# Kernel optimization log

Hardware: AMD Instinct MI355X
Metric: run time of the kernel (lower is better)

The kernel has to match this reference:

```python
import jax, jax.numpy as jnp
import numpy as np

MUL = 128            # channel multiplicity (node feature channels)
Z = 10               # number of chemical elements (node_attrs dim)
L_DIMS = (1, 3, 5, 7)   # edge SH irrep dims, lmax=3
MM_DIMS = (1, 3)        # magmom SH irrep dims, lmax=1
AVG_NUM_NEIGHBORS = 20.0
N_NODES = 5000
N_EDGES = 100000
R_DIM = 8            # edge radial feature dim
MM_INV_DIM = 8       # magmom invariant feature dim


def _mlp(x, Ws, act):
    # e3nn FullyConnectedNet: variance-preserving linear layers, act between hidden layers
    for W in Ws[:-1]:
        h = x @ W * (1.0 / np.sqrt(W.shape[0]))
        x = act(h) if act is not None else h
    return x @ Ws[-1] * (1.0 / np.sqrt(Ws[-1].shape[0]))


def _conv_tp(x, sh, w, dims):
    # channelwise 'uvu' tensor product: (MUL x 0e) x SH(l) -> MUL x l per l.
    # x:[E,MUL], sh:[E,sum(dims)], w:[E,MUL,n_l]. CG for 0e x l -> l is trivial.
    outs, off = [], 0
    for l, d in enumerate(dims):
        blk = (w[:, :, l] * x)[:, :, None] * sh[:, None, off:off + d]  # [E,MUL,d]
        outs.append(blk.reshape(x.shape[0], MUL * d))
        off += d
    return jnp.concatenate(outs, axis=-1)


def _per_l_linear(x, Ws, dims):
    # e3nn o3.Linear: per-l channel mixing with 1/sqrt(fan_in) normalization
    outs, off = [], 0
    scale = 1.0 / np.sqrt(MUL)
    for l, d in enumerate(dims):
        blk = x[:, off:off + MUL * d].reshape(-1, MUL, d)
        outs.append((jnp.einsum('nud,uv->nvd', blk, Ws[l]) * scale).reshape(-1, MUL * d))
        off += MUL * d
    return jnp.concatenate(outs, axis=-1)


def _skip_tp(x, attrs, Ws, dims):
    # FullyConnectedTensorProduct(irreps_out, Zx0e, irreps_out): per-l bilinear mix
    outs, off = [], 0
    scale = 1.0 / np.sqrt(MUL * attrs.shape[-1])
    for l, d in enumerate(dims):
        blk = x[:, off:off + MUL * d].reshape(-1, MUL, d)
        outs.append((jnp.einsum('nud,nz,uzv->nvd', blk, attrs, Ws[l]) * scale).reshape(-1, MUL * d))
        off += MUL * d
    return jnp.concatenate(outs, axis=-1)


def _reshape_irreps(x, dims):
    # [N, sum(MUL*d)] -> [N, MUL, sum(d)]
    outs, off = [], 0
    for d in dims:
        outs.append(x[:, off:off + MUL * d].reshape(-1, MUL, d))
        off += MUL * d
    return jnp.concatenate(outs, axis=-1)


def setup_inputs() -> dict:
    key = jax.random.key(0)
    ks = jax.random.split(key, 24)
    E, N = N_EDGES, N_NODES
    inp = {
        'node_attrs': jax.random.uniform(ks[0], (N, Z), jnp.float32),
        'node_feats': jax.random.normal(ks[1], (N, MUL), jnp.float32),
        'edge_attrs': jax.random.normal(ks[2], (E, sum(L_DIMS)), jnp.float32),
        'edge_feats': jax.random.uniform(ks[3], (E, R_DIM), jnp.float32),
        'magmom_node_inv_feats': jax.random.normal(ks[4], (N, MM_INV_DIM), jnp.float32),
        'magmom_node_attrs': jax.random.normal(ks[5], (N, sum(MM_DIMS)), jnp.float32),
        'edge_index': jax.random.randint(ks[6], (2, E), 0, N),
    }
    rin = R_DIM + MM_INV_DIM
    inp['W_up'] = jax.random.normal(ks[7], (MUL, MUL), jnp.float32)
    inp['W_rad1'] = jax.random.normal(ks[8], (rin, 64), jnp.float32)
    inp['W_rad2'] = jax.random.normal(ks[9], (64, 64), jnp.float32)
    inp['W_rad3'] = jax.random.normal(ks[10], (64, 64), jnp.float32)
    inp['W_rad4'] = jax.random.normal(ks[11], (64, MUL * len(L_DIMS)), jnp.float32)  # weight_numel=512
    inp['M_rad1'] = jax.random.normal(ks[12], (rin, 64), jnp.float32)
    inp['M_rad2'] = jax.random.normal(ks[13], (64, 64), jnp.float32)
    inp['M_rad3'] = jax.random.normal(ks[14], (64, 64), jnp.float32)
    inp['M_rad4'] = jax.random.normal(ks[15], (64, MUL * len(MM_DIMS)), jnp.float32)  # weight_numel=256
    inp['W_density'] = jax.random.normal(ks[16], (R_DIM, 1), jnp.float32)
    inp['W_lin'] = jax.random.normal(ks[17], (len(L_DIMS), MUL, MUL), jnp.float32)
    inp['W_mlin'] = jax.random.normal(ks[18], (len(MM_DIMS), MUL, MUL), jnp.float32)
    inp['W_skip'] = jax.random.normal(ks[19], (len(L_DIMS), MUL, Z, MUL), jnp.float32)
    inp['W_mskip'] = jax.random.normal(ks[20], (len(L_DIMS), MUL, Z, MUL), jnp.float32)
    return inp


def reference(node_attrs, node_feats, edge_attrs, edge_feats, magmom_node_inv_feats,
              magmom_node_attrs, W_up, W_rad1, W_rad2, W_rad3, W_rad4,
              M_rad1, M_rad2, M_rad3, M_rad4, W_density, W_lin, W_mlin,
              W_skip, W_mskip, edge_index):
    sender, receiver = edge_index[0], edge_index[1]
    E = edge_attrs.shape[0]
    N = node_feats.shape[0]
    silu = jax.nn.silu

    x = node_feats @ W_up * (1.0 / np.sqrt(MUL))  # linear_up
    xj = x[sender]                                # [E, MUL]
    ef_mm = jnp.concatenate([edge_feats, magmom_node_inv_feats[sender]], axis=-1)  # [E, 16]

    tp_w = _mlp(ef_mm, [W_rad1, W_rad2, W_rad3, W_rad4], silu)          # [E, 512]
    edge_density = jnp.tanh((edge_feats @ W_density * (1.0 / np.sqrt(R_DIM))) ** 2)  # [E, 1]

    w4 = tp_w.reshape(E, MUL, len(L_DIMS))
    pre_mji = _conv_tp(xj, edge_attrs, w4, L_DIMS)                      # [E, 2048]

    w_mm = _mlp(ef_mm, [M_rad1, M_rad2, M_rad3, M_rad4], None).reshape(E, MUL, len(MM_DIMS))
    w_mm = w_mm * pre_mji[:, :MUL][:, :, None]                          # density-gated by scalar part
    magmom_mji = _conv_tp(xj, magmom_node_attrs[sender], w_mm, MM_DIMS) # [E, 512]

    w4b = w4 * magmom_mji[:, :MUL][:, :, None]
    mji = _conv_tp(xj, edge_attrs, w4b, L_DIMS)                         # [E, 2048]

    density = jax.ops.segment_sum(edge_density, receiver, num_segments=N)  # [N, 1]
    msg = jax.ops.segment_sum(mji, receiver, num_segments=N)               # [N, 2048]
    mm_msg = jax.ops.segment_sum(magmom_mji, receiver, num_segments=N)     # [N, 512]

    msg = _per_l_linear(msg, W_lin, L_DIMS) / (density + 1.0)
    msg = _skip_tp(msg, node_attrs, W_skip, L_DIMS)

    mm = _per_l_linear(mm_msg, W_mlin, MM_DIMS) / AVG_NUM_NEIGHBORS
    # magmom_linear maps (128x0e+128x1o) -> target irreps: l=2,3 outputs have no path -> zero
    mm = jnp.concatenate([mm, jnp.zeros((N, MUL * (5 + 7)), mm.dtype)], axis=-1)
    mm = _skip_tp(mm, node_attrs, W_mskip, L_DIMS)

    out1 = _reshape_irreps(msg, L_DIMS)  # [N, 128, 16]
    out2 = _reshape_irreps(mm, L_DIMS)   # [N, 128, 16]
    return jnp.stack([out1, out2], axis=0)
```

## Files before the change

### kernel.cpp

```cpp
#include <hip/hip_runtime.h>
#include <stdint.h>


__device__ __forceinline__ float silu_f(float x) {
  return x / (1.0f + __expf(-x));
}

__global__ void k_zero_int(int* p, int n) {
  int i = blockIdx.x * blockDim.x + threadIdx.x;
  if (i < n) p[i] = 0;
}

__global__ __launch_bounds__(256) void k_prep(
    const float* __restrict__ M1, const float* __restrict__ M2,
    const float* __restrict__ M3, const float* __restrict__ M4,
    float* __restrict__ Mc) {
  __shared__ float T1[16 * 64];
  __shared__ float T2[16 * 64];
  int t = threadIdx.x;
  for (int i = t; i < 16 * 64; i += 256) {
    int r = i >> 6, c = i & 63;
    float s = 0.f;
    for (int k = 0; k < 64; k++) s += M1[r * 64 + k] * M2[k * 64 + c];
    T1[i] = s;
  }
// ... 56 lines not shown
    cursor[i] = base;
    base += deg[i];
  }
  if (t == 1023) rowstart[Nn] = part[1023];
}

__global__ void k_fill(const int* __restrict__ recv, int* __restrict__ cursor,
                       int* __restrict__ elist, int E) {
  int e = blockIdx.x * blockDim.x + threadIdx.x;
  if (e < E) {
    int p = atomicAdd(&cursor[recv[e]], 1);
    elist[p] = e;
  }
}

__global__ __launch_bounds__(256) void k_edge(
    const float* __restrict__ edge_feats, const float* __restrict__ mminv,
    const int* __restrict__ sender,
    const float* __restrict__ W1, const float* __restrict__ W2,
    const float* __restrict__ W3, const float* __restrict__ W4,
    const float* __restrict__ Mc, const float* __restrict__ Wd,
    float* __restrict__ w4e, float* __restrict__ wmme, float* __restrict__ dens,
    int E) {
  const int base = blockIdx.x * 8;
  const int t = threadIdx.x;
  __shared__ float ef[8][16];
  __shared__ float hA[8][64];
  __shared__ float hB[8][64];
  const int gwave = t >> 6;
  const int o6 = t & 63;

  if (t < 128) {
    int g = t >> 4, j = t & 15;
    int e = base + g;
    float v = 0.f;
    if (e < E) v = (j < 8) ? edge_feats[e * 8 + j] : mminv[sender[e] * 8 + (j - 8)];
    ef[g][j] = v;
  } else if (t < 136) {
    int g = t - 128;
    int e = base + g;
    if (e < E) {
      float q = 0.f;
#pragma unroll
      for (int k = 0; k < 8; k++) q += edge_feats[e * 8 + k] * Wd[k];
      q *= 0.35355339059327373f;
      dens[e] = tanhf(q * q);
    }
  }
  __syncthreads();

#pragma unroll
  for (int rep = 0; rep < 2; rep++) {
    int g = gwave + rep * 4;
    float s = 0.f;
#pragma unroll
    for (int k = 0; k < 16; k++) s += ef[g][k] * W1[k * 64 + o6];
// ... 31 lines not shown
    }
  }
  float c[8] = {0, 0, 0, 0, 0, 0, 0, 0};
#pragma unroll
  for (int k = 0; k < 16; k++) {
    float w = Mc[k * 256 + t];
#pragma unroll
    for (int g = 0; g < 8; g++) c[g] += ef[g][k] * w;
  }

  const int p0 = (t & 3) * 128 + (t >> 2);
  const int p1 = p0 + 64;
  const int pm = (t & 1) * 128 + (t >> 1);
#pragma unroll
  for (int g = 0; g < 8; g++) {
    int e = base + g;
    if (e < E) {
      w4e[(size_t)e * 512 + p0] = a[g] * 0.125f;
      w4e[(size_t)e * 512 + p1] = b[g] * 0.125f;
      wmme[(size_t)e * 256 + pm] = c[g];
    }
  }
}

__global__ __launch_bounds__(256) void k_edge_hA(
    const float* __restrict__ edge_feats, const float* __restrict__ mminv,
    const int* __restrict__ sender,
    const float* __restrict__ W1, const float* __restrict__ W2,
    const float* __restrict__ W3, const float* __restrict__ Wd,
    float* __restrict__ hAe, float* __restrict__ dens, int E) {
  const int base = blockIdx.x * 8;
  const int t = threadIdx.x;
  __shared__ float ef[8][16];
  __shared__ float hA[8][64];
  __shared__ float hB[8][64];
  const int gwave = t >> 6;
  const int o6 = t & 63;

  if (t < 128) {
    int g = t >> 4, j = t & 15;
    int e = base + g;
    float v = 0.f;
    if (e < E) v = (j < 8) ? edge_feats[e * 8 + j] : mminv[sender[e] * 8 + (j - 8)];
    ef[g][j] = v;
  } else if (t < 136) {
    int g = t - 128;
    int e = base + g;
    if (e < E) {
      float q = 0.f;
#pragma unroll
      for (int k = 0; k < 8; k++) q += edge_feats[e * 8 + k] * Wd[k];
      q *= 0.35355339059327373f;
      dens[e] = tanhf(q * q);
    }
  }
  __syncthreads();

#pragma unroll
  for (int rep = 0; rep < 2; rep++) {
    int g = gwave + rep * 4;
    float s = 0.f;
#pragma unroll
    for (int k = 0; k < 16; k++) s += ef[g][k] * W1[k * 64 + o6];
    hA[g][o6] = silu_f(s * 0.25f);
  }
#pragma unroll
  for (int rep = 0; rep < 2; rep++) {
    int g = gwave + rep * 4;
    float s = 0.f;
#pragma unroll 8
    for (int k = 0; k < 64; k++) s += hA[g][k] * W2[k * 64 + o6];
    hB[g][o6] = silu_f(s * 0.125f);
  }
#pragma unroll
  for (int rep = 0; rep < 2; rep++) {
    int g = gwave + rep * 4;
    float s = 0.f;
#pragma unroll 8
    for (int k = 0; k < 64; k++) s += hB[g][k] * W3[k * 64 + o6];
    int e = base + g;
    if (e < E) hAe[(size_t)e * 64 + o6] = silu_f(s * 0.125f);
  }
}

__global__ __launch_bounds__(256) void k_gather0(
    const float* __restrict__ x, const float* __restrict__ edge_attrs,
    const float* __restrict__ mmattrs, const int* __restrict__ sender,
    const float* __restrict__ w4e, const float* __restrict__ wmme,
    const float* __restrict__ dens,
    const int* __restrict__ rowstart, const int* __restrict__ elist,
    float* __restrict__ msg, float* __restrict__ mmr, float* __restrict__ densN,
    int Nn) {
  const int n = blockIdx.x;
  const int t = threadIdx.x;
  const int start = rowstart[n], end = rowstart[n + 1];

  __shared__ float shs[2][8][16];
  __shared__ float mmshs[2][8][4];

  float accm[8] = {0, 0, 0, 0, 0, 0, 0, 0};
  float accmm0 = 0.f, accmm1 = 0.f, accd = 0.f;
  const int u = t & 127;
  const int half = t >> 7;

  int erA[8], srA[8], erB[8], srB[8];
#pragma unroll
  for (int g = 0; g < 8; g++) { erA[g] = -1; srA[g] = 0; erB[g] = -1; srB[g] = 0; }

  if (start < end) {
    int idx = start + (t & 7);
    int v = (idx < end) ? elist[idx] : -1;
    int s = (v >= 0) ? sender[v] : 0;
    float d = (v >= 0) ? dens[v] : 0.f;
#pragma unroll
    for (int g = 0; g < 8; g++) {
      erA[g] = __shfl(v, g);
      srA[g] = __shfl(s, g);
      float dg = __shfl(d, g);
      if (t == 0) accd += dg;
    }
    if (t < 128) {
      int g = t >> 4, j = t & 15;
      shs[0][g][j] = (erA[g] >= 0) ? edge_attrs[erA[g] * 16 + j] : 0.f;
    } else if (t < 160) {
// ... 14 lines not shown
#pragma unroll
      for (int g = 0; g < 8; g++) {
        erB[g] = __shfl(v, g);
        srB[g] = __shfl(s, g);
        float dg = __shfl(d, g);
        if (t == 0) accd += dg;
      }
      if (t < 128) {
        int g = t >> 4, j = t & 15;
        shs[p ^ 1][g][j] = (erB[g] >= 0) ? edge_attrs[erB[g] * 16 + j] : 0.f;
      } else if (t < 160) {
        int g = (t - 128) >> 2, j = (t - 128) & 3;
        mmshs[p ^ 1][g][j] = (erB[g] >= 0) ? mmattrs[srB[g] * 4 + j] : 0.f;
      }
    }
#pragma unroll 2
    for (int g = 0; g < 8; g++) {
      if (erA[g] < 0) continue;
      const size_t b4 = (size_t)erA[g] * 512;
      const size_t bm = (size_t)erA[g] * 256;
      float w40 = w4e[b4 + u];
      float w41 = w4e[b4 + 128 + u];
      float w42 = w4e[b4 + 256 + u];
      float w43 = w4e[b4 + 384 + u];
      float wm0 = wmme[bm + u];
      float wm1 = wmme[bm + 128 + u];
      float xj = x[(size_t)srA[g] * 128 + u];
      float sh0 = shs[p][g][0];
      float pre0 = w40 * xj * sh0;
      float wg0 = wm0 * pre0;
      float wg1 = wm1 * pre0;
      float mm0 = wg0 * xj * mmshs[p][g][0];
      float m1 = wg1 * xj;
      float bx = mm0 * xj;
      float b0 = w40 * bx, b1 = w41 * bx, b2 = w42 * bx, b3 = w43 * bx;
      if (half == 0) {
        accmm0 += mm0;
        accmm1 += m1 * mmshs[p][g][1];
        accm[0] += b0 * sh0;
        accm[1] += b1 * shs[p][g][1];
        accm[2] += b1 * shs[p][g][2];
// ... 10 lines not shown
        accm[2] += b3 * shs[p][g][10];
        accm[3] += b3 * shs[p][g][11];
        accm[4] += b3 * shs[p][g][12];
        accm[5] += b3 * shs[p][g][13];
        accm[6] += b3 * shs[p][g][14];
        accm[7] += b3 * shs[p][g][15];
      }
    }
    __syncthreads();
    p ^= 1;
#pragma unroll
    for (int g = 0; g < 8; g++) { erA[g] = erB[g]; srA[g] = srB[g]; }
  }

  float4* mp = (float4*)(msg + (size_t)n * 2048 + u * 16 + half * 8);
  mp[0] = make_float4(accm[0], accm[1], accm[2], accm[3]);
  mp[1] = make_float4(accm[4], accm[5], accm[6], accm[7]);
  *(float2*)(mmr + (size_t)n * 512 + u * 4 + half * 2) = make_float2(accmm0, accmm1);
  if (t == 0) densN[n] = accd;
}

template <int D, int SP>
__device__ __forceinline__ void lin_body(
    const float* __restrict__ in, int in_rs, int in_us, int in_cb,
    const float* __restrict__ W, const float* __restrict__ densN, float basescl,
    bool useDinv, float* __restrict__ outp, int out_rs, int out_us, int out_cb,
    int Nn, int n0, float* lin_s) {
  const int t = threadIdx.x;
  for (int i = t; i < 16 * 128 * D; i += 256) {
    int nn = i / (128 * D);
    int r = i - nn * 128 * D;
    int uu = r / D;
    int m = r - uu * D;
    int nd = n0 + nn;
    lin_s[(nn * 128 + uu) * SP + m] =
        (nd < Nn) ? in[(size_t)nd * in_rs + uu * in_us + in_cb + m] : 0.f;
  }
  __syncthreads();

  const int v = t & 127, hf = t >> 7;
  float acc[8][D];
#pragma unroll
  for (int q = 0; q < 8; q++)
#pragma unroll
    for (int m = 0; m < D; m++) acc[q][m] = 0.f;

  for (int uu = 0; uu < 128; uu++) {
    float wv = W[uu * 128 + v];
#pragma unroll
    for (int q = 0; q < 8; q++) {
      const float* ls = &lin_s[((hf * 8 + q) * 128 + uu) * SP];
#pragma unroll
      for (int m = 0; m < D; m++) acc[q][m] += ls[m] * wv;
    }
  }
#pragma unroll
  for (int q = 0; q < 8; q++) {
    int nd = n0 + hf * 8 + q;
    if (nd < Nn) {
      float scl = basescl;
      if (useDinv) scl *= 1.0f / (densN[nd] + 1.0f);
      float* op = outp + (size_t)nd * out_rs + v * out_us + out_cb;
#pragma unroll
      for (int m = 0; m < D; m++) op[m] = acc[q][m] * scl;
    }
  }
}

__global__ __launch_bounds__(256) void k_lin(
    const float* __restrict__ msg, const float* __restrict__ mmr,
    const float* __restrict__ densN, const float* __restrict__ Wlin,
    const float* __restrict__ Wmlin, float* __restrict__ linm,
    float* __restrict__ linmm, int Nn) {
  __shared__ float lin_s[16 * 128 * 8];
  const int n0 = blockIdx.x * 16;
  const float scl = 0.08838834764831845f;
  const float sm = 0.08838834764831845f / 20.0f;
  switch (blockIdx.y) {
    case 0: lin_body<1, 1>(msg, 2048, 16, 0, Wlin, densN, scl, true, linm, 2048, 16, 0, Nn, n0, lin_s); break;
    case 1: lin_body<3, 4>(msg, 2048, 16, 1, Wlin + 16384, densN, scl, true, linm, 2048, 16, 1, Nn, n0, lin_s); break;
    case 2: lin_body<5, 8>(msg, 2048, 16, 4, Wlin + 32768, densN, scl, true, linm, 2048, 16, 4, Nn, n0, lin_s); break;
    case 3: lin_body<7, 8>(msg, 2048, 16, 9, Wlin + 49152, densN, scl, true, linm, 2048, 16, 9, Nn, n0, lin_s); break;
    case 4: lin_body<1, 1>(mmr, 512, 4, 0, Wmlin, densN, sm, false, linmm, 512, 4, 0, Nn, n0, lin_s); break;
    case 5: lin_body<3, 4>(mmr, 512, 4, 1, Wmlin + 16384, densN, sm, false, linmm, 512, 4, 1, Nn, n0, lin_s); break;
  }
}

template <int MODE>
__global__ __launch_bounds__(256) void k_gather_t(
    const float* __restrict__ x, const float* __restrict__ edge_attrs,
    const float* __restrict__ edge_feats, const float* __restrict__ mminv,
    const float* __restrict__ mmattrs, const int* __restrict__ sender,
    const float* __restrict__ W1, const float* __restrict__ W2,
    const float* __restrict__ W3, const float* __restrict__ W4,
    const float* __restrict__ Mc, const float* __restrict__ Wd,
    const float* __restrict__ dens, const float* __restrict__ hAe,
    const float* __restrict__ Wlin, const float* __restrict__ Wmlin,
    const int* __restrict__ rowstart, const int* __restrict__ elist,
    float* __restrict__ linm, float* __restrict__ linmm, int Nn) {
  const int n = blockIdx.x;
  const int t = threadIdx.x;
  const int start = rowstart[n], end = rowstart[n + 1];

  __shared__ float ef[8][16];
  __shared__ float hA[8][64];
  __shared__ float hB[8][64];
  __shared__ float ubuf[8 * 512 + 8 * 256];
  __shared__ float xjs[8][128];
  __shared__ float shs[8][16];
  __shared__ float mmshs[8][4];
  __shared__ float denss[8];
// ... 9 lines not shown
  float accmm0 = 0.f, accmm1 = 0.f;
  float accd = 0.f;

  const int u = t & 127;
  const int half = t >> 7;
  const int gwave = t >> 6;
  const int o6 = t & 63;

  for (int base = start; base < end; base += 8) {
    if (t < 8) {
      int g = t;
      if (base + g < end) {
        int e = elist[base + g];
        eS[g] = e;
        sS[g] = sender[e];
        if (MODE == 1) denss[g] = dens[e];
      } else {
        eS[g] = -1;
        sS[g] = 0;
        denss[g] = 0.f;
      }
    }
    __syncthreads();
    if (t < 128) {
      int g = t >> 4, j = t & 15;
      int e = eS[g];
      shs[g][j] = (e >= 0) ? edge_attrs[e * 16 + j] : 0.f;
      float v = 0.f;
      if (e >= 0) v = (j < 8) ? edge_feats[e * 8 + j] : mminv[sS[g] * 8 + (j - 8)];
      ef[g][j] = v;
    } else if (t < 160) {
      int g = (t - 128) >> 2, j = (t - 128) & 3;
      mmshs[g][j] = (eS[g] >= 0) ? mmattrs[sS[g] * 4 + j] : 0.f;
    }
    for (int i = t; i < 1024; i += 256) {
      int g = i >> 7, uu = i & 127;
      xjs[g][uu] = (eS[g] >= 0) ? x[sS[g] * 128 + uu] : 0.f;
    }
    if constexpr (MODE == 1) {
      for (int i = t; i < 512; i += 256) {
        int g = i >> 6, k = i & 63;
        hA[g][k] = (eS[g] >= 0) ? hAe[(size_t)eS[g] * 64 + k] : 0.f;
      }
    }
    if constexpr (MODE == 2) {
      if (t < 8 && eS[t] >= 0) {
        int e = eS[t];
        float q = 0.f;
#pragma unroll
        for (int k = 0; k < 8; k++) q += edge_feats[e * 8 + k] * Wd[k];
        q *= 0.35355339059327373f;
        denss[t] = tanhf(q * q);
      }
    }
    __syncthreads();

    if constexpr (MODE == 2) {
#pragma unroll
      for (int rep = 0; rep < 2; rep++) {
        int g = gwave + rep * 4;
        float s = 0.f;
#pragma unroll
        for (int k = 0; k < 16; k++) s += ef[g][k] * W1[k * 64 + o6];
        hA[g][o6] = silu_f(s * 0.25f);
      }
#pragma unroll
      for (int rep = 0; rep < 2; rep++) {
        int g = gwave + rep * 4;
        float s = 0.f;
#pragma unroll 8
        for (int k = 0; k < 64; k++) s += hA[g][k] * W2[k * 64 + o6];
        hB[g][o6] = silu_f(s * 0.125f);
      }
#pragma unroll
      for (int rep = 0; rep < 2; rep++) {
        int g = gwave + rep * 4;
        float s = 0.f;
#pragma unroll 8
        for (int k = 0; k < 64; k++) s += hB[g][k] * W3[k * 64 + o6];
        hA[g][o6] = silu_f(s * 0.125f);
      }
      __syncthreads();
    }

    {
      float a[8] = {0, 0, 0, 0, 0, 0, 0, 0};
      float b[8] = {0, 0, 0, 0, 0, 0, 0, 0};
#pragma unroll 8
      for (int k = 0; k < 64; k++) {
        float w0 = W4[k * 512 + t];
        float w1 = W4[k * 512 + t + 256];
#pragma unroll
        for (int g = 0; g < 8; g++) {
          float h = hA[g][k];
          a[g] += h * w0;
          b[g] += h * w1;
        }
      }
      int p0 = (t & 3) * 128 + (t >> 2);
// ... 5 lines not shown
      }
    }
    {
      float c[8] = {0, 0, 0, 0, 0, 0, 0, 0};
#pragma unroll
      for (int k = 0; k < 16; k++) {
        float w = Mc[k * 256 + t];
#pragma unroll
        for (int g = 0; g < 8; g++) c[g] += ef[g][k] * w;
      }
      int p = (t & 1) * 128 + (t >> 1);
#pragma unroll
      for (int g = 0; g < 8; g++) wmms[g][p] = c[g];
    }
    __syncthreads();

#pragma unroll 2
    for (int g = 0; g < 8; g++) {
      float w40 = w4s[g][u];
      float w41 = w4s[g][128 + u];
      float w42 = w4s[g][256 + u];
      float w43 = w4s[g][384 + u];
      float wm0 = wmms[g][u];
      float wm1 = wmms[g][128 + u];
      float xj = xjs[g][u];
      float sh0 = shs[g][0];
      float pre0 = w40 * xj * sh0;
      float wg0 = wm0 * pre0;
      float wg1 = wm1 * pre0;
      float mm0 = wg0 * xj * mmshs[g][0];
      float m1 = wg1 * xj;
      float bx = mm0 * xj;
      float b0 = w40 * bx, b1 = w41 * bx, b2 = w42 * bx, b3 = w43 * bx;
      if (half == 0) {
        accmm0 += mm0;
        accmm1 += m1 * mmshs[g][1];
        accm[0] += b0 * sh0;
        accm[1] += b1 * shs[g][1];
        accm[2] += b1 * shs[g][2];
        accm[3] += b1 * shs[g][3];
        accm[4] += b2 * shs[g][4];
        accm[5] += b2 * shs[g][5];
        accm[6] += b2 * shs[g][6];
        accm[7] += b2 * shs[g][7];
// ... 42 lines not shown
    }
  } else {
    for (int uu = 0; uu < 128; uu++) {
      float wl2 = Wlin[32768 + uu * 128 + u];
      float wl3 = Wlin[49152 + uu * 128 + u];
      outl[0] += msg_s[uu][8] * wl2;
      outl[1] += msg_s[uu][9] * wl3;
      outl[2] += msg_s[uu][10] * wl3;
      outl[3] += msg_s[uu][11] * wl3;
      outl[4] += msg_s[uu][12] * wl3;
      outl[5] += msg_s[uu][13] * wl3;
      outl[6] += msg_s[uu][14] * wl3;
      outl[7] += msg_s[uu][15] * wl3;
    }
  }
  const float scl = 0.08838834764831845f * dinv;
  float4 v0 = make_float4(outl[0] * scl, outl[1] * scl, outl[2] * scl, outl[3] * scl);
  float4 v1 = make_float4(outl[4] * scl, outl[5] * scl, outl[6] * scl, outl[7] * scl);
  float4* lp = (float4*)(linm + (size_t)n * 2048 + u * 16 + half * 8);
  lp[0] = v0;
  lp[1] = v1;

  float om0 = 0.f, om1 = 0.f;
  if (half == 0) {
    for (int uu = 0; uu < 128; uu++) {
      om0 += mm_s[uu][0] * Wmlin[uu * 128 + u];
      om1 += mm_s[uu][1] * Wmlin[16384 + uu * 128 + u];
    }
  } else {
    for (int uu = 0; uu < 128; uu++) {
      float wm1 = Wmlin[16384 + uu * 128 + u];
      om0 += mm_s[uu][2] * wm1;
      om1 += mm_s[uu][3] * wm1;
    }
  }
  const float sm = 0.08838834764831845f / 20.0f;
  *(float2*)(linmm + (size_t)n * 512 + u * 4 + half * 2) = make_float2(om0 * sm, om1 * sm);
}

__global__ void k_zero2(float* __restrict__ out2, int Nn) {
  int i = blockIdx.x * blockDim.x + threadIdx.x;
  if (i < Nn * 128) {
    float4 z = make_float4(0.f, 0.f, 0.f, 0.f);
    float4* p = (float4*)(out2 + (size_t)i * 16);
    p[1] = z;
    p[2] = z;
    p[3] = z;
  }
}

__global__ __launch_bounds__(128) void k_wt(const float* __restrict__ Wskip,
                                            const float* __restrict__ Wmskip,
                                            float* __restrict__ Wt) {
  int bx = blockIdx.x;
  int L = bx >> 7, u = bx & 127;
  int v = threadIdx.x;
  const float* src = (L < 4) ? (Wskip + (size_t)L * 163840)
                             : (Wmskip + (size_t)(L - 4) * 163840);
  float* dst = Wt + (((size_t)L * 128 + u) * 128 + v) * 12;
#pragma unroll
  for (int z = 0; z < 10; z++) dst[z] = src[u * 1280 + z * 128 + v];
  dst[10] = 0.f;
  dst[11] = 0.f;
}

template <int D, int SP>
__device__ __forceinline__ void skip_body2(
    const float* __restrict__ attrs, const float* __restrict__ in, int in_rs,
    int in_us, int in_cb, const float* __restrict__ Wt, float* __restrict__ outp,
    int out_cb, int Nn, int n0, float* lin_s, float (*attrs_s)[10]) {
  const int t = threadIdx.x;
  for (int i = t; i < 160; i += 256) {
    int nn = i / 10, z = i - nn * 10;
    int n = n0 + nn;
    attrs_s[nn][z] = (n < Nn) ? attrs[n * 10 + z] : 0.f;
  }
  for (int i = t; i < 16 * 128 * D; i += 256) {
    int nn = i / (128 * D);
// ... 85 lines not shown
  const float* M2 = (const float*)d_in[13];
  const float* M3 = (const float*)d_in[14];
  const float* M4 = (const float*)d_in[15];
  const float* Wd = (const float*)d_in[16];
  const float* Wlin = (const float*)d_in[17];
  const float* Wmlin = (const float*)d_in[18];
  const float* Wskip = (const float*)d_in[19];
  const float* Wmskip = (const float*)d_in[20];

  const int N = in_sizes[1] / 128;
  const int E = in_sizes[2] / 16;
  const int* sender = edge_index;
  const int* recv = edge_index + E;

  float* ws = (float*)d_ws;
  float* x = ws;   ws += (size_t)N * 128;
  float* Mc = ws;  ws += 16 * 256;
  float* Wt = ws;  ws += (size_t)6 * 128 * 128 * 12;

  const size_t intWords = (size_t)(N + 1) + N + N + E;
  const size_t headBytes = (size_t)((char*)ws - (char*)d_ws);
  const size_t needA = headBytes +
      ((size_t)N * 2048 + (size_t)N * 512 + N + intWords +
       (size_t)E * 512 + (size_t)E * 256 + E) * 4 + 64;
  const size_t needB = headBytes +
      ((size_t)N * 2048 + (size_t)N * 512 + (size_t)E * 64 + E + intWords) * 4 + 64;

  int mode;
  float *msg = nullptr, *mmr = nullptr, *densN = nullptr;
  float *w4e = nullptr, *wmme = nullptr, *dens = nullptr, *hAe = nullptr;
  float *linm = nullptr, *linmm = nullptr;
  int* ibuf = nullptr;

  if (ws_size >= needA) {
    mode = 0;
    msg = ws;   ws += (size_t)N * 2048;
    mmr = ws;   ws += (size_t)N * 512;
    densN = ws; ws += N;
    ibuf = (int*)ws;
    ws = (float*)(((uintptr_t)(ibuf + intWords) + 15) & ~(uintptr_t)15);
    w4e = ws;   ws += (size_t)E * 512;
    wmme = ws;  ws += (size_t)E * 256;
    dens = ws;  ws += E;
    linm = w4e;
    linmm = w4e + (size_t)N * 2048;
  } else if (ws_size >= needB) {
    mode = 1;
    linm = ws;  ws += (size_t)N * 2048;
    linmm = ws; ws += (size_t)N * 512;
    hAe = ws;   ws += (size_t)E * 64;
    dens = ws;  ws += E;
    ibuf = (int*)ws;
  } else {
    mode = 2;
    linm = ws;  ws += (size_t)N * 2048;
    linmm = ws; ws += (size_t)N * 512;
    ibuf = (int*)ws;
  }
  int* rowstart = ibuf;
  int* deg = ibuf + (N + 1);
  int* cursor = deg + N;
  int* elist = cursor + N;

  k_zero_int<<<(N + 255) / 256, 256, 0, stream>>>(deg, N);
  k_prep<<<1, 256, 0, stream>>>(M1, M2, M3, M4, Mc);
  k_wt<<<768, 128, 0, stream>>>(Wskip, Wmskip, Wt);
  k_up<<<N, 128, 0, stream>>>(node_feats, W_up, x, N);
  if (mode == 0) {
    k_edge<<<(E + 7) / 8, 256, 0, stream>>>(edge_feats, mminv, sender, W1, W2,
                                            W3, W4, Mc, Wd, w4e, wmme, dens, E);
  } else if (mode == 1) {
    k_edge_hA<<<(E + 7) / 8, 256, 0, stream>>>(edge_feats, mminv, sender, W1,
                                               W2, W3, Wd, hAe, dens, E);
  }
  k_count<<<(E + 255) / 256, 256, 0, stream>>>(recv, deg, E);
  k_scan<<<1, 1024, 0, stream>>>(deg, rowstart, cursor, N);
  k_fill<<<(E + 255) / 256, 256, 0, stream>>>(recv, cursor, elist, E);
  dim3 gs((N + 15) / 16, 6);
  if (mode == 0) {
    k_gather0<<<N, 256, 0, stream>>>(x, edge_attrs, mmattrs, sender, w4e, wmme,
                                     dens, rowstart, elist, msg, mmr, densN, N);
    k_lin<<<gs, 256, 0, stream>>>(msg, mmr, densN, Wlin, Wmlin, linm, linmm, N);
  } else if (mode == 1) {
    k_gather_t<1><<<N, 256, 0, stream>>>(x, edge_attrs, edge_feats, mminv,
                                         mmattrs, sender, W1, W2, W3, W4, Mc,
                                         Wd, dens, hAe, Wlin, Wmlin, rowstart,
                                         elist, linm, linmm, N);
  } else {
    k_gather_t<2><<<N, 256, 0, stream>>>(x, edge_attrs, edge_feats, mminv,
                                         mmattrs, sender, W1, W2, W3, W4, Mc,
                                         Wd, dens, hAe, Wlin, Wmlin, rowstart,
                                         elist, linm, linmm, N);
  }
  k_zero2<<<(N * 128 + 255) / 256, 256, 0, stream>>>((float*)d_out + (size_t)N * 2048, N);
  k_skip<<<gs, 256, 0, stream>>>(node_attrs, linm, linmm, Wt, (float*)d_out, N);
}
```

Baseline: 978.8 us.

## Compute edge weights in receiver-sorted segments and fuse linear into skip kernel

Edge weights are now computed in receiver-sorted order over segments sized to fit the workspace. A gather kernel runs per segment and accumulates into node buffers, replacing the earlier three workspace-dependent modes. The per-l linear is fused into the skip tensor-product kernel, which removes the intermediate linm/linmm buffers and one kernel launch. The gather now reads edge weights contiguously instead of scattering by edge id, at the cost of read-modify-write accumulation, an extra zeroing pass and possibly several segment launches.

```diff
diff --git a/kernel.cpp b/kernel.cpp
--- a/kernel.cpp
+++ b/kernel.cpp
@@ -9,6 +9,11 @@
 __global__ void k_zero_int(int* p, int n) {
   int i = blockIdx.x * blockDim.x + threadIdx.x;
   if (i < n) p[i] = 0;
+}
+
+__global__ void k_zero_f(float* p, int n) {
+  int i = blockIdx.x * blockDim.x + threadIdx.x;
+  if (i < n) p[i] = 0.f;
 }
 
 __global__ __launch_bounds__(256) void k_prep(
@@ -95,32 +100,35 @@
   }
 }
 
-__global__ __launch_bounds__(256) void k_edge(
+__global__ __launch_bounds__(256) void k_edge_pos(
     const float* __restrict__ edge_feats, const float* __restrict__ mminv,
-    const int* __restrict__ sender,
+    const int* __restrict__ sender, const int* __restrict__ elist,
     const float* __restrict__ W1, const float* __restrict__ W2,
     const float* __restrict__ W3, const float* __restrict__ W4,
     const float* __restrict__ Mc, const float* __restrict__ Wd,
-    float* __restrict__ w4e, float* __restrict__ wmme, float* __restrict__ dens,
-    int E) {
-  const int base = blockIdx.x * 8;
+    float* __restrict__ w4p, float* __restrict__ wmmp, float* __restrict__ dens,
+    int plo, int phi) {
+  const int base = plo + blockIdx.x * 8;
   const int t = threadIdx.x;
+  __shared__ int eS[8];
   __shared__ float ef[8][16];
   __shared__ float hA[8][64];
   __shared__ float hB[8][64];
   const int gwave = t >> 6;
   const int o6 = t & 63;
 
+  if (t < 8) eS[t] = (base + t < phi) ? elist[base + t] : -1;
+  __syncthreads();
   if (t < 128) {
     int g = t >> 4, j = t & 15;
-    int e = base + g;
+    int e = eS[g];
     float v = 0.f;
-    if (e < E) v = (j < 8) ? edge_feats[e * 8 + j] : mminv[sender[e] * 8 + (j - 8)];
+    if (e >= 0) v = (j < 8) ? edge_feats[e * 8 + j] : mminv[sender[e] * 8 + (j - 8)];
     ef[g][j] = v;
   } else if (t < 136) {
     int g = t - 128;
-    int e = base + g;
-    if (e < E) {
+    int e = eS[g];
+    if (e >= 0) {
       float q = 0.f;
 #pragma unroll
       for (int k = 0; k < 8; k++) q += edge_feats[e * 8 + k] * Wd[k];
@@ -182,86 +190,29 @@
   const int pm = (t & 1) * 128 + (t >> 1);
 #pragma unroll
   for (int g = 0; g < 8; g++) {
-    int e = base + g;
-    if (e < E) {
-      w4e[(size_t)e * 512 + p0] = a[g] * 0.125f;
-      w4e[(size_t)e * 512 + p1] = b[g] * 0.125f;
-      wmme[(size_t)e * 256 + pm] = c[g];
-    }
-  }
-}
-
-__global__ __launch_bounds__(256) void k_edge_hA(
-    const float* __restrict__ edge_feats, const float* __restrict__ mminv,
-    const int* __restrict__ sender,
-    const float* __restrict__ W1, const float* __restrict__ W2,
-    const float* __restrict__ W3, const float* __restrict__ Wd,
-    float* __restrict__ hAe, float* __restrict__ dens, int E) {
-  const int base = blockIdx.x * 8;
-  const int t = threadIdx.x;
-  __shared__ float ef[8][16];
-  __shared__ float hA[8][64];
-  __shared__ float hB[8][64];
-  const int gwave = t >> 6;
-  const int o6 = t & 63;
-
-  if (t < 128) {
-    int g = t >> 4, j = t & 15;
-    int e = base + g;
-    float v = 0.f;
-    if (e < E) v = (j < 8) ? edge_feats[e * 8 + j] : mminv[sender[e] * 8 + (j - 8)];
-    ef[g][j] = v;
-  } else if (t < 136) {
-    int g = t - 128;
-    int e = base + g;
-    if (e < E) {
-      float q = 0.f;
-#pragma unroll
-      for (int k = 0; k < 8; k++) q += edge_feats[e * 8 + k] * Wd[k];
-      q *= 0.35355339059327373f;
-      dens[e] = tanhf(q * q);
-    }
-  }
-  __syncthreads();
-
-#pragma unroll
-  for (int rep = 0; rep < 2; rep++) {
-    int g = gwave + rep * 4;
-    float s = 0.f;
-#pragma unroll
-    for (int k = 0; k < 16; k++) s += ef[g][k] * W1[k * 64 + o6];
-    hA[g][o6] = silu_f(s * 0.25f);
-  }
-#pragma unroll
-  for (int rep = 0; rep < 2; rep++) {
-    int g = gwave + rep * 4;
-    float s = 0.f;
-#pragma unroll 8
-    for (int k = 0; k < 64; k++) s += hA[g][k] * W2[k * 64 + o6];
-    hB[g][o6] = silu_f(s * 0.125f);
-  }
-#pragma unroll
-  for (int rep = 0; rep < 2; rep++) {
-    int g = gwave + rep * 4;
-    float s = 0.f;
-#pragma unroll 8
-    for (int k = 0; k < 64; k++) s += hB[g][k] * W3[k * 64 + o6];
-    int e = base + g;
-    if (e < E) hAe[(size_t)e * 64 + o6] = silu_f(s * 0.125f);
-  }
-}
-
-__global__ __launch_bounds__(256) void k_gather0(
+    if (base + g < phi) {
+      size_t wb = (size_t)(base + g - plo);
+      w4p[wb * 512 + p0] = a[g] * 0.125f;
+      w4p[wb * 512 + p1] = b[g] * 0.125f;
+      wmmp[wb * 256 + pm] = c[g];
+    }
+  }
+}
+
+__global__ __launch_bounds__(256) void k_gather_seg(
     const float* __restrict__ x, const float* __restrict__ edge_attrs,
     const float* __restrict__ mmattrs, const int* __restrict__ sender,
-    const float* __restrict__ w4e, const float* __restrict__ wmme,
+    const float* __restrict__ w4p, const float* __restrict__ wmmp,
     const float* __restrict__ dens,
     const int* __restrict__ rowstart, const int* __restrict__ elist,
     float* __restrict__ msg, float* __restrict__ mmr, float* __restrict__ densN,
-    int Nn) {
+    int plo, int phi, int Nn) {
   const int n = blockIdx.x;
   const int t = threadIdx.x;
-  const int start = rowstart[n], end = rowstart[n + 1];
+  int s0 = rowstart[n], s1 = rowstart[n + 1];
+  int start = s0 > plo ? s0 : plo;
+  int end = s1 < phi ? s1 : phi;
+  if (start >= end) return;
 
   __shared__ float shs[2][8][16];
   __shared__ float mmshs[2][8][4];
@@ -275,7 +226,7 @@
 #pragma unroll
   for (int g = 0; g < 8; g++) { erA[g] = -1; srA[g] = 0; erB[g] = -1; srB[g] = 0; }
 
-  if (start < end) {
+  {
     int idx = start + (t & 7);
     int v = (idx < end) ? elist[idx] : -1;
     int s = (v >= 0) ? sender[v] : 0;
@@ -320,17 +271,18 @@
         mmshs[p ^ 1][g][j] = (erB[g] >= 0) ? mmattrs[srB[g] * 4 + j] : 0.f;
       }
     }
+    const size_t wbase = (size_t)(base - plo);
 #pragma unroll 2
     for (int g = 0; g < 8; g++) {
       if (erA[g] < 0) continue;
-      const size_t b4 = (size_t)erA[g] * 512;
-      const size_t bm = (size_t)erA[g] * 256;
-      float w40 = w4e[b4 + u];
-      float w41 = w4e[b4 + 128 + u];
-      float w42 = w4e[b4 + 256 + u];
-      float w43 = w4e[b4 + 384 + u];
-      float wm0 = wmme[bm + u];
-      float wm1 = wmme[bm + 128 + u];
+      const float* w4g = w4p + (wbase + g) * 512;
+      const float* wmg = wmmp + (wbase + g) * 256;
+      float w40 = w4g[u];
+      float w41 = w4g[128 + u];
+      float w42 = w4g[256 + u];
+      float w43 = w4g[384 + u];
+      float wm0 = wmg[u];
+      float wm1 = wmg[128 + u];
       float xj = x[(size_t)srA[g] * 128 + u];
       float sh0 = shs[p][g][0];
       float pre0 = w40 * xj * sh0;
@@ -371,87 +323,166 @@
   }
 
   float4* mp = (float4*)(msg + (size_t)n * 2048 + u * 16 + half * 8);
-  mp[0] = make_float4(accm[0], accm[1], accm[2], accm[3]);
-  mp[1] = make_float4(accm[4], accm[5], accm[6], accm[7]);
-  *(float2*)(mmr + (size_t)n * 512 + u * 4 + half * 2) = make_float2(accmm0, accmm1);
-  if (t == 0) densN[n] = accd;
+  float4 o0 = mp[0], o1 = mp[1];
+  o0.x += accm[0]; o0.y += accm[1]; o0.z += accm[2]; o0.w += accm[3];
+  o1.x += accm[4]; o1.y += accm[5]; o1.z += accm[6]; o1.w += accm[7];
+  mp[0] = o0;
+  mp[1] = o1;
+  float2* m2 = (float2*)(mmr + (size_t)n * 512 + u * 4 + half * 2);
+  float2 om = *m2;
+  om.x += accmm0;
+  om.y += accmm1;
+  *m2 = om;
+  if (t == 0) densN[n] += accd;
+}
+
+__global__ void k_zero2(float* __restrict__ out2, int Nn) {
+  int i = blockIdx.x * blockDim.x + threadIdx.x;
+  if (i < Nn * 128) {
+    float4 z = make_float4(0.f, 0.f, 0.f, 0.f);
+    float4* p = (float4*)(out2 + (size_t)i * 16);
+    p[1] = z;
+    p[2] = z;
+    p[3] = z;
+  }
+}
+
+__global__ __launch_bounds__(128) void k_wt(const float* __restrict__ Wskip,
+                                            const float* __restrict__ Wmskip,
+                                            float* __restrict__ Wt) {
+  int bx = blockIdx.x;
+  int L = bx >> 7, u = bx & 127;
+  int v = threadIdx.x;
+  const float* src = (L < 4) ? (Wskip + (size_t)L * 163840)
+                             : (Wmskip + (size_t)(L - 4) * 163840);
+  float* dst = Wt + (((size_t)L * 128 + u) * 128 + v) * 12;
+#pragma unroll
+  for (int z = 0; z < 10; z++) dst[z] = src[u * 1280 + z * 128 + v];
+  dst[10] = 0.f;
+  dst[11] = 0.f;
 }
 
 template <int D, int SP>
-__device__ __forceinline__ void lin_body(
-    const float* __restrict__ in, int in_rs, int in_us, int in_cb,
-    const float* __restrict__ W, const float* __restrict__ densN, float basescl,
-    bool useDinv, float* __restrict__ outp, int out_rs, int out_us, int out_cb,
-    int Nn, int n0, float* lin_s) {
+__device__ __forceinline__ void skip2_body(
+    const float* __restrict__ attrs, const float* __restrict__ in, int in_rs,
+    int in_us, int in_cb, const float* __restrict__ Wl,
+    const float* __restrict__ densN, float basescl, bool useDinv,
+    const float* __restrict__ Wt, float* __restrict__ outp, int out_cb,
+    int Nn, int n0, float* lin_s, float (*attrs_s)[10]) {
   const int t = threadIdx.x;
+  for (int i = t; i < 160; i += 256) {
+    int nn = i / 10, z = i - nn * 10;
+    int n = n0 + nn;
+    attrs_s[nn][z] = (n < Nn) ? attrs[n * 10 + z] : 0.f;
+  }
   for (int i = t; i < 16 * 128 * D; i += 256) {
     int nn = i / (128 * D);
     int r = i - nn * 128 * D;
     int uu = r / D;
     int m = r - uu * D;
-    int nd = n0 + nn;
+    int n = n0 + nn;
     lin_s[(nn * 128 + uu) * SP + m] =
-        (nd < Nn) ? in[(size_t)nd * in_rs + uu * in_us + in_cb + m] : 0.f;
+        (n < Nn) ? in[(size_t)n * in_rs + uu * in_us + in_cb + m] : 0.f;
   }
   __syncthreads();
 
   const int v = t & 127, hf = t >> 7;
-  float acc[8][D];
+
+  float lm[8][D];
 #pragma unroll
   for (int q = 0; q < 8; q++)
 #pragma unroll
-    for (int m = 0; m < D; m++) acc[q][m] = 0.f;
-
+    for (int m = 0; m < D; m++) lm[q][m] = 0.f;
   for (int uu = 0; uu < 128; uu++) {
-    float wv = W[uu * 128 + v];
+    float wv = Wl[uu * 128 + v];
 #pragma unroll
     for (int q = 0; q < 8; q++) {
       const float* ls = &lin_s[((hf * 8 + q) * 128 + uu) * SP];
 #pragma unroll
-      for (int m = 0; m < D; m++) acc[q][m] += ls[m] * wv;
-    }
-  }
+      for (int m = 0; m < D; m++) lm[q][m] += ls[m] * wv;
+    }
+  }
+  __syncthreads();
 #pragma unroll
   for (int q = 0; q < 8; q++) {
     int nd = n0 + hf * 8 + q;
-    if (nd < Nn) {
-      float scl = basescl;
-      if (useDinv) scl *= 1.0f / (densN[nd] + 1.0f);
-      float* op = outp + (size_t)nd * out_rs + v * out_us + out_cb;
-#pragma unroll
-      for (int m = 0; m < D; m++) op[m] = acc[q][m] * scl;
-    }
-  }
-}
-
-__global__ __launch_bounds__(256) void k_lin(
-    const float* __restrict__ msg, const float* __restrict__ mmr,
-    const float* __restrict__ densN, const float* __restrict__ Wlin,
-    const float* __restrict__ Wmlin, float* __restrict__ linm,
-    float* __restrict__ linmm, int Nn) {
+    float scl = basescl;
+    if (useDinv) scl *= 1.0f / (((nd < Nn) ? densN[nd] : 0.f) + 1.0f);
+    float* ls = &lin_s[((hf * 8 + q) * 128 + v) * SP];
+#pragma unroll
+    for (int m = 0; m < D; m++) ls[m] = lm[q][m] * scl;
+  }
+  __syncthreads();
+
+  float ar[8][10];
+#pragma unroll
+  for (int q = 0; q < 8; q++)
+#pragma unroll
+    for (int z = 0; z < 10; z++) ar[q][z] = attrs_s[hf * 8 + q][z];
+
+  float acc[8][D];
+#pragma unroll
+  for (int q = 0; q < 8; q++)
+#pragma unroll
+    for (int m = 0; m < D; m++) acc[q][m] = 0.f;
+
+  const float* wp0 = Wt + (size_t)v * 12;
+  for (int u = 0; u < 128; u++) {
+    const float* wp = wp0 + (size_t)u * 1536;
+    float4 wa = *(const float4*)wp;
+    float4 wb = *(const float4*)(wp + 4);
+    float2 wc = *(const float2*)(wp + 8);
+    float wr[10] = {wa.x, wa.y, wa.z, wa.w, wb.x, wb.y, wb.z, wb.w, wc.x, wc.y};
+#pragma unroll
+    for (int q = 0; q < 8; q++) {
+      float wn = 0.f;
+#pragma unroll
+      for (int z = 0; z < 10; z++) wn += ar[q][z] * wr[z];
+      const float* ls = &lin_s[((hf * 8 + q) * 128 + u) * SP];
+#pragma unroll
+      for (int m = 0; m < D; m++) acc[q][m] += ls[m] * wn;
+    }
+  }
+#pragma unroll
+  for (int q = 0; q < 8; q++) {
+    int n = n0 + hf * 8 + q;
+    if (n < Nn) {
+      float* op = outp + (size_t)n * 2048 + v * 16 + out_cb;
+#pragma unroll
+      for (int m = 0; m < D; m++) op[m] = acc[q][m] * 0.027950849718747371f;
+    }
+  }
+}
+
+__global__ __launch_bounds__(256) void k_skip2(
+    const float* __restrict__ attrs, const float* __restrict__ msg,
+    const float* __restrict__ mmr, const float* __restrict__ densN,
+    const float* __restrict__ Wlin, const float* __restrict__ Wmlin,
+    const float* __restrict__ Wt, float* __restrict__ out, int Nn) {
   __shared__ float lin_s[16 * 128 * 8];
+  __shared__ float attrs_s[16][10];
   const int n0 = blockIdx.x * 16;
+  const int job = blockIdx.y;
+  const float* Wtj = Wt + (size_t)job * 128 * 128 * 12;
   const float scl = 0.08838834764831845f;
   const float sm = 0.08838834764831845f / 20.0f;
-  switch (blockIdx.y) {
-    case 0: lin_body<1, 1>(msg, 2048, 16, 0, Wlin, densN, scl, true, linm, 2048, 16, 0, Nn, n0, lin_s); break;
-    case 1: lin_body<3, 4>(msg, 2048, 16, 1, Wlin + 16384, densN, scl, true, linm, 2048, 16, 1, Nn, n0, lin_s); break;
-    case 2: lin_body<5, 8>(msg, 2048, 16, 4, Wlin + 32768, densN, scl, true, linm, 2048, 16, 4, Nn, n0, lin_s); break;
-    case 3: lin_body<7, 8>(msg, 2048, 16, 9, Wlin + 49152, densN, scl, true, linm, 2048, 16, 9, Nn, n0, lin_s); break;
-    case 4: lin_body<1, 1>(mmr, 512, 4, 0, Wmlin, densN, sm, false, linmm, 512, 4, 0, Nn, n0, lin_s); break;
-    case 5: lin_body<3, 4>(mmr, 512, 4, 1, Wmlin + 16384, densN, sm, false, linmm, 512, 4, 1, Nn, n0, lin_s); break;
-  }
-}
-
-template <int MODE>
-__global__ __launch_bounds__(256) void k_gather_t(
+  switch (job) {
+    case 0: skip2_body<1, 1>(attrs, msg, 2048, 16, 0, Wlin, densN, scl, true, Wtj, out, 0, Nn, n0, lin_s, attrs_s); break;
+    case 1: skip2_body<3, 4>(attrs, msg, 2048, 16, 1, Wlin + 16384, densN, scl, true, Wtj, out, 1, Nn, n0, lin_s, attrs_s); break;
+    case 2: skip2_body<5, 8>(attrs, msg, 2048, 16, 4, Wlin + 32768, densN, scl, true, Wtj, out, 4, Nn, n0, lin_s, attrs_s); break;
+    case 3: skip2_body<7, 8>(attrs, msg, 2048, 16, 9, Wlin + 49152, densN, scl, true, Wtj, out, 9, Nn, n0, lin_s, attrs_s); break;
+    case 4: skip2_body<1, 1>(attrs, mmr, 512, 4, 0, Wmlin, densN, sm, false, Wtj, out + (size_t)Nn * 2048, 0, Nn, n0, lin_s, attrs_s); break;
+    case 5: skip2_body<3, 4>(attrs, mmr, 512, 4, 1, Wmlin + 16384, densN, sm, false, Wtj, out + (size_t)Nn * 2048, 1, Nn, n0, lin_s, attrs_s); break;
+  }
+}
+
+__global__ __launch_bounds__(256) void k_gather_f(
     const float* __restrict__ x, const float* __restrict__ edge_attrs,
     const float* __restrict__ edge_feats, const float* __restrict__ mminv,
     const float* __restrict__ mmattrs, const int* __restrict__ sender,
     const float* __restrict__ W1, const float* __restrict__ W2,
     const float* __restrict__ W3, const float* __restrict__ W4,
     const float* __restrict__ Mc, const float* __restrict__ Wd,
-    const float* __restrict__ dens, const float* __restrict__ hAe,
     const float* __restrict__ Wlin, const float* __restrict__ Wmlin,
     const int* __restrict__ rowstart, const int* __restrict__ elist,
     float* __restrict__ linm, float* __restrict__ linmm, int Nn) {
@@ -491,7 +522,6 @@
         int e = elist[base + g];
         eS[g] = e;
         sS[g] = sender[e];
-        if (MODE == 1) denss[g] = dens[e];
       } else {
         eS[g] = -1;
         sS[g] = 0;
@@ -514,52 +544,41 @@
       int g = i >> 7, uu = i & 127;
       xjs[g][uu] = (eS[g] >= 0) ? x[sS[g] * 128 + uu] : 0.f;
     }
-    if constexpr (MODE == 1) {
-      for (int i = t; i < 512; i += 256) {
-        int g = i >> 6, k = i & 63;
-        hA[g][k] = (eS[g] >= 0) ? hAe[(size_t)eS[g] * 64 + k] : 0.f;
-      }
-    }
-    if constexpr (MODE == 2) {
-      if (t < 8 && eS[t] >= 0) {
-        int e = eS[t];
-        float q = 0.f;
-#pragma unroll
-        for (int k = 0; k < 8; k++) q += edge_feats[e * 8 + k] * Wd[k];
-        q *= 0.35355339059327373f;
-        denss[t] = tanhf(q * q);
-      }
+    if (t < 8 && eS[t] >= 0) {
+      int e = eS[t];
+      float q = 0.f;
+#pragma unroll
+      for (int k = 0; k < 8; k++) q += edge_feats[e * 8 + k] * Wd[k];
+      q *= 0.35355339059327373f;
+      denss[t] = tanhf(q * q);
     }
     __syncthreads();
 
-    if constexpr (MODE == 2) {
-#pragma unroll
-      for (int rep = 0; rep < 2; rep++) {
-        int g = gwave + rep * 4;
-        float s = 0.f;
-#pragma unroll
-        for (int k = 0; k < 16; k++) s += ef[g][k] * W1[k * 64 + o6];
-        hA[g][o6] = silu_f(s * 0.25f);
-      }
-#pragma unroll
-      for (int rep = 0; rep < 2; rep++) {
-        int g = gwave + rep * 4;
-        float s = 0.f;
+#pragma unroll
+    for (int rep = 0; rep < 2; rep++) {
+      int g = gwave + rep * 4;
+      float s = 0.f;
+#pragma unroll
+      for (int k = 0; k < 16; k++) s += ef[g][k] * W1[k * 64 + o6];
+      hA[g][o6] = silu_f(s * 0.25f);
+    }
+#pragma unroll
+    for (int rep = 0; rep < 2; rep++) {
+      int g = gwave + rep * 4;
+      float s = 0.f;
 #pragma unroll 8
-        for (int k = 0; k < 64; k++) s += hA[g][k] * W2[k * 64 + o6];
-        hB[g][o6] = silu_f(s * 0.125f);
-      }
-#pragma unroll
-      for (int rep = 0; rep < 2; rep++) {
-        int g = gwave + rep * 4;
-        float s = 0.f;
+      for (int k = 0; k < 64; k++) s += hA[g][k] * W2[k * 64 + o6];
+      hB[g][o6] = silu_f(s * 0.125f);
+    }
+#pragma unroll
+    for (int rep = 0; rep < 2; rep++) {
+      int g = gwave + rep * 4;
+      float s = 0.f;
 #pragma unroll 8
-        for (int k = 0; k < 64; k++) s += hB[g][k] * W3[k * 64 + o6];
-        hA[g][o6] = silu_f(s * 0.125f);
-      }
-      __syncthreads();
-    }
-
+      for (int k = 0; k < 64; k++) s += hB[g][k] * W3[k * 64 + o6];
+      hA[g][o6] = silu_f(s * 0.125f);
+    }
+    __syncthreads();
     {
       float a[8] = {0, 0, 0, 0, 0, 0, 0, 0};
       float b[8] = {0, 0, 0, 0, 0, 0, 0, 0};
@@ -595,20 +614,17 @@
       for (int g = 0; g < 8; g++) wmms[g][p] = c[g];
     }
     __syncthreads();
-
 #pragma unroll 2
     for (int g = 0; g < 8; g++) {
+      float xj = xjs[g][u];
+      float sh0 = shs[g][0];
       float w40 = w4s[g][u];
       float w41 = w4s[g][128 + u];
       float w42 = w4s[g][256 + u];
       float w43 = w4s[g][384 + u];
-      float wm0 = wmms[g][u];
-      float wm1 = wmms[g][128 + u];
-      float xj = xjs[g][u];
-      float sh0 = shs[g][0];
       float pre0 = w40 * xj * sh0;
-      float wg0 = wm0 * pre0;
-      float wg1 = wm1 * pre0;
+      float wg0 = wmms[g][u] * pre0;
+      float wg1 = wmms[g][128 + u] * pre0;
       float mm0 = wg0 * xj * mmshs[g][0];
       float m1 = wg1 * xj;
       float bx = mm0 * xj;
@@ -681,9 +697,9 @@
       outl[7] += msg_s[uu][15] * wl3;
     }
   }
-  const float scl = 0.08838834764831845f * dinv;
-  float4 v0 = make_float4(outl[0] * scl, outl[1] * scl, outl[2] * scl, outl[3] * scl);
-  float4 v1 = make_float4(outl[4] * scl, outl[5] * scl, outl[6] * scl, outl[7] * scl);
+  const float sclv = 0.08838834764831845f * dinv;
+  float4 v0 = make_float4(outl[0] * sclv, outl[1] * sclv, outl[2] * sclv, outl[3] * sclv);
+  float4 v1 = make_float4(outl[4] * sclv, outl[5] * sclv, outl[6] * sclv, outl[7] * sclv);
   float4* lp = (float4*)(linm + (size_t)n * 2048 + u * 16 + half * 8);
   lp[0] = v0;
   lp[1] = v1;
@@ -703,32 +719,6 @@
   }
   const float sm = 0.08838834764831845f / 20.0f;
   *(float2*)(linmm + (size_t)n * 512 + u * 4 + half * 2) = make_float2(om0 * sm, om1 * sm);
-}
-
-__global__ void k_zero2(float* __restrict__ out2, int Nn) {
-  int i = blockIdx.x * blockDim.x + threadIdx.x;
-  if (i < Nn * 128) {
-    float4 z = make_float4(0.f, 0.f, 0.f, 0.f);
-    float4* p = (float4*)(out2 + (size_t)i * 16);
-    p[1] = z;
-    p[2] = z;
-    p[3] = z;
-  }
-}
-
-__global__ __launch_bounds__(128) void k_wt(const float* __restrict__ Wskip,
-                                            const float* __restrict__ Wmskip,
-                                            float* __restrict__ Wt) {
-  int bx = blockIdx.x;
-  int L = bx >> 7, u = bx & 127;
-  int v = threadIdx.x;
-  const float* src = (L < 4) ? (Wskip + (size_t)L * 163840)
-                             : (Wmskip + (size_t)(L - 4) * 163840);
-  float* dst = Wt + (((size_t)L * 128 + u) * 128 + v) * 12;
-#pragma unroll
-  for (int z = 0; z < 10; z++) dst[z] = src[u * 1280 + z * 128 + v];
-  dst[10] = 0.f;
-  dst[11] = 0.f;
 }
 
 template <int D, int SP>
@@ -844,84 +834,57 @@
   const int* recv = edge_index + E;
 
   float* ws = (float*)d_ws;
-  float* x = ws;   ws += (size_t)N * 128;
-  float* Mc = ws;  ws += 16 * 256;
-  float* Wt = ws;  ws += (size_t)6 * 128 * 128 * 12;
-
-  const size_t intWords = (size_t)(N + 1) + N + N + E;
-  const size_t headBytes = (size_t)((char*)ws - (char*)d_ws);
-  const size_t needA = headBytes +
-      ((size_t)N * 2048 + (size_t)N * 512 + N + intWords +
-       (size_t)E * 512 + (size_t)E * 256 + E) * 4 + 64;
-  const size_t needB = headBytes +
-      ((size_t)N * 2048 + (size_t)N * 512 + (size_t)E * 64 + E + intWords) * 4 + 64;
-
-  int mode;
-  float *msg = nullptr, *mmr = nullptr, *densN = nullptr;
-  float *w4e = nullptr, *wmme = nullptr, *dens = nullptr, *hAe = nullptr;
-  float *linm = nullptr, *linmm = nullptr;
-  int* ibuf = nullptr;
-
-  if (ws_size >= needA) {
-    mode = 0;
-    msg = ws;   ws += (size_t)N * 2048;
-    mmr = ws;   ws += (size_t)N * 512;
-    densN = ws; ws += N;
-    ibuf = (int*)ws;
-    ws = (float*)(((uintptr_t)(ibuf + intWords) + 15) & ~(uintptr_t)15);
-    w4e = ws;   ws += (size_t)E * 512;
-    wmme = ws;  ws += (size_t)E * 256;
-    dens = ws;  ws += E;
-    linm = w4e;
-    linmm = w4e + (size_t)N * 2048;
-  } else if (ws_size >= needB) {
-    mode = 1;
-    linm = ws;  ws += (size_t)N * 2048;
-    linmm = ws; ws += (size_t)N * 512;
-    hAe = ws;   ws += (size_t)E * 64;
-    dens = ws;  ws += E;
-    ibuf = (int*)ws;
-  } else {
-    mode = 2;
-    linm = ws;  ws += (size_t)N * 2048;
-    linmm = ws; ws += (size_t)N * 512;
-    ibuf = (int*)ws;
-  }
+  float* x = ws;     ws += (size_t)N * 128;
+  float* Mc = ws;    ws += 16 * 256;
+  float* Wt = ws;    ws += (size_t)6 * 128 * 128 * 12;
+  float* msg = ws;   ws += (size_t)N * 2048;
+  float* mmr = ws;   ws += (size_t)N * 512;
+  float* densN = ws; ws += N;
+  float* dens = ws;  ws += E;
+  int* ibuf = (int*)ws;
   int* rowstart = ibuf;
   int* deg = ibuf + (N + 1);
   int* cursor = deg + N;
   int* elist = cursor + N;
+  float* segbase = (float*)(((uintptr_t)(elist + E) + 63) & ~(uintptr_t)63);
+  size_t usedBytes = (size_t)((char*)segbase - (char*)d_ws);
+  size_t budgetW = (ws_size > usedBytes + 256) ? (ws_size - usedBytes - 256) / 4 : 0;
+  size_t sege = (budgetW / 768) & ~(size_t)7;
+  if (sege > (size_t)E) sege = ((size_t)E + 7) & ~(size_t)7;
+  const bool mainPath = sege >= 64;
+  float* w4p = segbase;
+  float* wmmp = segbase + sege * 512;
 
   k_zero_int<<<(N + 255) / 256, 256, 0, stream>>>(deg, N);
   k_prep<<<1, 256, 0, stream>>>(M1, M2, M3, M4, Mc);
   k_wt<<<768, 128, 0, stream>>>(Wskip, Wmskip, Wt);
   k_up<<<N, 128, 0, stream>>>(node_feats, W_up, x, N);
-  if (mode == 0) {
-    k_edge<<<(E + 7) / 8, 256, 0, stream>>>(edge_feats, mminv, sender, W1, W2,
-                                            W3, W4, Mc, Wd, w4e, wmme, dens, E);
-  } else if (mode == 1) {
-    k_edge_hA<<<(E + 7) / 8, 256, 0, stream>>>(edge_feats, mminv, sender, W1,
-                                               W2, W3, Wd, hAe, dens, E);
-  }
   k_count<<<(E + 255) / 256, 256, 0, stream>>>(recv, deg, E);
   k_scan<<<1, 1024, 0, stream>>>(deg, rowstart, cursor, N);
   k_fill<<<(E + 255) / 256, 256, 0, stream>>>(recv, cursor, elist, E);
+
   dim3 gs((N + 15) / 16, 6);
-  if (mode == 0) {
-    k_gather0<<<N, 256, 0, stream>>>(x, edge_attrs, mmattrs, sender, w4e, wmme,
-                                     dens, rowstart, elist, msg, mmr, densN, N);
-    k_lin<<<gs, 256, 0, stream>>>(msg, mmr, densN, Wlin, Wmlin, linm, linmm, N);
-  } else if (mode == 1) {
-    k_gather_t<1><<<N, 256, 0, stream>>>(x, edge_attrs, edge_feats, mminv,
-                                         mmattrs, sender, W1, W2, W3, W4, Mc,
-                                         Wd, dens, hAe, Wlin, Wmlin, rowstart,
-                                         elist, linm, linmm, N);
+  if (mainPath) {
+    const int zn = N * 2048 + N * 512 + N;
+    k_zero_f<<<(zn + 255) / 256, 256, 0, stream>>>(msg, zn);
+    for (int plo = 0; plo < E; plo += (int)sege) {
+      int phi = plo + (int)sege;
+      if (phi > E) phi = E;
+      k_edge_pos<<<(phi - plo + 7) / 8, 256, 0, stream>>>(
+          edge_feats, mminv, sender, elist, W1, W2, W3, W4, Mc, Wd, w4p, wmmp,
+          dens, plo, phi);
+      k_gather_seg<<<N, 256, 0, stream>>>(x, edge_attrs, mmattrs, sender, w4p,
+                                          wmmp, dens, rowstart, elist, msg,
+                                          mmr, densN, plo, phi, N);
+    }
+    k_zero2<<<(N * 128 + 255) / 256, 256, 0, stream>>>((float*)d_out + (size_t)N * 2048, N);
+    k_skip2<<<gs, 256, 0, stream>>>(node_attrs, msg, mmr, densN, Wlin, Wmlin,
+                                    Wt, (float*)d_out, N);
   } else {
-    k_gather_t<2><<<N, 256, 0, stream>>>(x, edge_attrs, edge_feats, mminv,
-                                         mmattrs, sender, W1, W2, W3, W4, Mc,
-                                         Wd, dens, hAe, Wlin, Wmlin, rowstart,
-                                         elist, linm, linmm, N);
-  }
-  k_zero2<<<(N * 128 + 255) / 256, 256, 0, stream>>>((float*)d_out + (size_t)N * 2048, N);
-  k_skip<<<gs, 256, 0, stream>>>(node_attrs, linm, linmm, Wt, (float*)d_out, N);
-}
+    k_gather_f<<<N, 256, 0, stream>>>(x, edge_attrs, edge_feats, mminv,
+                                      mmattrs, sender, W1, W2, W3, W4, Mc, Wd,
+                                      Wlin, Wmlin, rowstart, elist, msg, mmr, N);
+    k_zero2<<<(N * 128 + 255) / 256, 256, 0, stream>>>((float*)d_out + (size_t)N * 2048, N);
+    k_skip<<<gs, 256, 0, stream>>>(node_attrs, msg, mmr, Wt, (float*)d_out, N);
+  }
+}
```

Measured after the change: 1.144 ms. 1.17x slower.
